# Kernel tuning notes

Hardware: AMD Instinct MI355X
Metric: run time of the kernel (lower is better)

Reference implementation:

```python
import jax, jax.numpy as jnp
import numpy as np

N_EMBD = 512  # scale uses C = n_embd, per original code

def setup_inputs() -> dict:
    key = jax.random.key(0)
    k1, k2, k3, k4 = jax.random.split(key, 4)
    B, T, C, H = 4, 4096, N_EMBD, 64
    x = jax.random.normal(k1, (B, T, C), dtype=jnp.float32)
    # Linear(n_embd, head_size, bias=False); stored as [C, H] for x @ W
    scale = 1.0 / np.sqrt(C)
    Wq = jax.random.normal(k2, (C, H), dtype=jnp.float32) * scale
    Wk = jax.random.normal(k3, (C, H), dtype=jnp.float32) * scale
    Wv = jax.random.normal(k4, (C, H), dtype=jnp.float32) * scale
    return {"x": x, "Wq": Wq, "Wk": Wk, "Wv": Wv}

def reference(x, Wq, Wk, Wv):
    B, T, C = x.shape
    q = jnp.einsum('btc,ch->bth', x, Wq)
    k = jnp.einsum('btc,ch->bth', x, Wk)
    v = jnp.einsum('btc,ch->bth', x, Wv)
    # NOTE: original scales by sqrt(C)=sqrt(n_embd), not sqrt(head_size)
    scores = jnp.einsum('bqh,bkh->bqk', q, k) / jnp.sqrt(jnp.float32(C))
    causal = jnp.tril(jnp.ones((T, T), dtype=bool))
    scores = jnp.where(causal, scores, -jnp.inf)
    weights = jax.nn.softmax(scores, axis=-1)
    out = jnp.einsum('bqk,bkh->bqh', weights, v)
    return out
```

## Files before the change

### kernel.cpp

```cpp
#include <hip/hip_runtime.h>

#define DEV __device__ __forceinline__

typedef __bf16 bf16x8 __attribute__((ext_vector_type(8)));
typedef unsigned short u16x8v __attribute__((ext_vector_type(8)));
typedef float f32x4 __attribute__((ext_vector_type(4)));
typedef float f32x16 __attribute__((ext_vector_type(16)));
typedef unsigned int u32x4v __attribute__((ext_vector_type(4)));
typedef unsigned short u16;
typedef unsigned int u32;

DEV u16 f2bf(float f) {
    u32 u = __builtin_bit_cast(u32, f);
    u = (u + 0x7FFFu + ((u >> 16) & 1u)) >> 16;
    return (u16)u;
}

DEV float bf2f(u16 v) {
    return __builtin_bit_cast(float, (u32)v << 16);
}

DEV bf16x8 ld_bf8(const u16* p) {
    return *reinterpret_cast<const bf16x8*>(p);
}

DEV bf16x8 ld_lds8(const u16* p) {
    ushort4 a = *reinterpret_cast<const ushort4*>(p);
    ushort4 b = *reinterpret_cast<const ushort4*>(p + 4);
    u16x8v o;
    o[0] = a.x; o[1] = a.y; o[2] = a.z; o[3] = a.w;
    o[4] = b.x; o[5] = b.y; o[6] = b.z; o[7] = b.w;
    return __builtin_bit_cast(bf16x8, o);
}

DEV float fexp2(float x) { return __builtin_amdgcn_exp2f(x); }

DEV u32 cvt_pk_bf16(float a, float b) {
    u32 r;
    asm("v_cvt_pk_bf16_f32 %0, %1, %2" : "=v"(r) : "v"(a), "v"(b));
    return r;
}


DEV int block_base(int j) {
    int g = j >> 1, r = j & 1;
    return j + g * (g - 1) + r * g;
}

__global__ __launch_bounds__(256) void prep_kernel(const float* __restrict__ W0,
                                                   const float* __restrict__ W1,
                                                   const float* __restrict__ W2,
                                                   u16* __restrict__ Wt,
                                                   u32* __restrict__ table) {
    const int blk = blockIdx.x;
    if (blk < 384) {
        int idx = blk * 256 + threadIdx.x;
        int w = idx >> 15, rem = idx & 32767, h = rem >> 9, c = rem & 511;
        const float* W = (w == 0) ? W0 : ((w == 1) ? W1 : W2);
        float v = W[c * 64 + h];
        if (w == 0) v *= 0.044194173824159216f * 1.4426950408889634f;
        Wt[idx] = f2bf(v);
    } else {
        int idx = (blk - 384) * 256 + threadIdx.x;
        if (idx < 512) {
            int j = idx >> 4, k = idx & 15;
            if (k <= (j >> 1))
                table[block_base(j) + k] = (u32)j | ((u32)k << 16);
        }
    }
}

__global__ __launch_bounds__(256) void proj_kernel(const float* __restrict__ x,
                                                   const u16* __restrict__ Wt,
                                                   u16* __restrict__ Q,
                                                   u16* __restrict__ Kq,
                                                   u16* __restrict__ Vt) {
    __shared__ __align__(16) u16 xs[64 * 40];
    const int tid = threadIdx.x;
    const int wave = tid >> 6, lane = tid & 63;
    const int lr = lane & 15, lg = lane >> 4;
    const int r0 = blockIdx.x * 64;
    const int srow = tid >> 3, scol = (tid & 7) * 4;

    f32x4 acc[3][4];
#pragma unroll
    for (int m = 0; m < 3; ++m)
#pragma unroll
        for (int b = 0; b < 4; ++b) acc[m][b] = (f32x4){0.f, 0.f, 0.f, 0.f};

    for (int kk = 0; kk < 16; ++kk) {
#pragma unroll
        for (int p = 0; p < 2; ++p) {
            const int row = p * 32 + srow;
            float4 a = *reinterpret_cast<const float4*>(
                x + (size_t)(r0 + row) * 512 + kk * 32 + scol);
            ushort4 hv;
            hv.x = f2bf(a.x); hv.y = f2bf(a.y); hv.z = f2bf(a.z); hv.w = f2bf(a.w);
            *reinterpret_cast<ushort4*>(&xs[row * 40 + scol]) = hv;
        }
        __syncthreads();

        bf16x8 af = ld_bf8(&xs[(wave * 16 + lr) * 40 + lg * 8]);
#pragma unroll
        for (int m = 0; m < 3; ++m) {
#pragma unroll
            for (int nt = 0; nt < 4; ++nt) {
                bf16x8 bf = ld_bf8(Wt + m * 32768 + (lr + 16 * nt) * 512 + kk * 32 + lg * 8);
                acc[m][nt] = __builtin_amdgcn_mfma_f32_16x16x32_bf16(af, bf, acc[m][nt], 0, 0, 0);
            }
        }
        __syncthreads();
    }

    const int rw = r0 + wave * 16;
#pragma unroll
    for (int nt = 0; nt < 4; ++nt) {
        const int h = lr + 16 * nt;
#pragma unroll
        for (int reg = 0; reg < 4; ++reg) {
            Q[(size_t)(rw + 4 * lg + reg) * 64 + h]  = f2bf(acc[0][nt][reg]);
            Kq[(size_t)(rw + 4 * lg + reg) * 64 + h] = f2bf(acc[1][nt][reg]);
        }
    }
    const int bidx = rw >> 12;
    const int t0 = (rw & 4095) + 4 * lg;
#pragma unroll
    for (int nt = 0; nt < 4; ++nt) {
        const int h = lr + 16 * nt;
        ushort4 hv;
        hv.x = f2bf(acc[2][nt][0]); hv.y = f2bf(acc[2][nt][1]);
        hv.z = f2bf(acc[2][nt][2]); hv.w = f2bf(acc[2][nt][3]);
        *reinterpret_cast<ushort4*>(Vt + ((size_t)(bidx * 64 + h)) * 4096 + t0) = hv;
    }
}

DEV void mask_diag(f32x16& st, int q31, int hi) {
#pragma unroll
    for (int reg = 0; reg < 16; ++reg) {
        const int crow = (reg & 3) + 8 * (reg >> 2) + 4 * hi;
        if (crow > q31) st[reg] = -3.0e38f;
    }
}

DEV float max16(const f32x16& a) {
    float m0 = fmaxf(fmaxf(a[0], a[1]), a[2]);
    float m1 = fmaxf(fmaxf(a[3], a[4]), a[5]);
    float m2 = fmaxf(fmaxf(a[6], a[7]), a[8]);
    float m3 = fmaxf(fmaxf(a[9], a[10]), a[11]);
    float m4 = fmaxf(fmaxf(a[12], a[13]), a[14]);
    float m5 = fmaxf(fmaxf(m0, m1), a[15]);
    float m6 = fmaxf(fmaxf(m2, m3), m4);
    return fmaxf(m5, m6);
}

DEV float expsum(f32x16& st, float m) {
    float r0 = 0.f, r1 = 0.f, r2 = 0.f, r3 = 0.f;
#pragma unroll
    for (int g = 0; g < 4; ++g) {
        float p0 = fexp2(st[4 * g + 0] - m);
        float p1 = fexp2(st[4 * g + 1] - m);
        float p2 = fexp2(st[4 * g + 2] - m);
        float p3 = fexp2(st[4 * g + 3] - m);
        st[4 * g + 0] = p0; st[4 * g + 1] = p1;
        st[4 * g + 2] = p2; st[4 * g + 3] = p3;
        r0 += p0; r1 += p1; r2 += p2; r3 += p3;
    }
    return (r0 + r1) + (r2 + r3);
}

DEV void packP(const f32x16& st, bf16x8& pb0, bf16x8& pb1, int hi) {
    u32 A0 = cvt_pk_bf16(st[0], st[1]),  A1 = cvt_pk_bf16(st[2], st[3]);
    u32 A2 = cvt_pk_bf16(st[4], st[5]),  A3 = cvt_pk_bf16(st[6], st[7]);
    u32 A4 = cvt_pk_bf16(st[8], st[9]),  A5 = cvt_pk_bf16(st[10], st[11]);
    u32 A6 = cvt_pk_bf16(st[12], st[13]), A7 = cvt_pk_bf16(st[14], st[15]);
    u32 e0 = __shfl_xor(hi ? A0 : A2, 32, 64);
    u32 e1 = __shfl_xor(hi ? A1 : A3, 32, 64);
    u32 e2 = __shfl_xor(hi ? A4 : A6, 32, 64);
    u32 e3 = __shfl_xor(hi ? A5 : A7, 32, 64);
    u32x4v w0, w1;
    w0[0] = hi ? e0 : A0;
    w0[1] = hi ? e1 : A1;
    w0[2] = hi ? A2 : e0;
    w0[3] = hi ? A3 : e1;
    w1[0] = hi ? e2 : A4;
    w1[1] = hi ? e3 : A5;
    w1[2] = hi ? A6 : e2;
    w1[3] = hi ? A7 : e3;
    pb0 = __builtin_bit_cast(bf16x8, w0);
    pb1 = __builtin_bit_cast(bf16x8, w1);
}

__global__ __launch_bounds__(256) void attn_part_kernel(const u16* __restrict__ Q,
                                                        const u16* __restrict__ K,
                                                        const u16* __restrict__ Vt,
                                                        const u32* __restrict__ table,
                                                        u16* __restrict__ Opart,
                                                        float* __restrict__ Mpart,
                                                        float* __restrict__ Lpart) {
    __shared__ __align__(16) u16 Ks[2][32][68];
    __shared__ __align__(16) u16 Vs[2][64][36];

    const int tid = threadIdx.x;
    const int wave = tid >> 6, lane = tid & 63;
    const int q31 = lane & 31, hi = lane >> 5;
    const int bid = blockIdx.x;
    const int b = bid & 3;
    const u32 e = table[bid >> 2];
    const int j = (int)(e & 0xffff);
    const int c = (int)(e >> 16);
    const int qi = 4 * j + wave;
    const int qr0 = qi * 32;
    const int s0 = c * 8;
    const int s1 = min(4 * j + 4, s0 + 8);
    const int tile = (b << 7) | qi;

    const u16* Qb = Q + (size_t)b * 4096 * 64;
    const u16* Kb = K + (size_t)b * 4096 * 64;
    const u16* Vb = Vt + (size_t)b * 64 * 4096;

    const int kr = tid >> 3, ku = tid & 7;
    const int vd = tid >> 2, vu = tid & 3;
    const u16* ksrc = Kb + (size_t)kr * 64 + ku * 8;
    const u16* vsrc = Vb + (size_t)vd * 4096 + vu * 8;

    bf16x8 qf[4];
#pragma unroll
    for (int kk = 0; kk < 4; ++kk)
        qf[kk] = ld_bf8(Qb + (size_t)(qr0 + q31) * 64 + kk * 16 + hi * 8);

    f32x16 o0, o1;
#pragma unroll
    for (int r = 0; r < 16; ++r) { o0[r] = 0.f; o1[r] = 0.f; }
    float m_run = -1.0e30f, l_run = 0.f;

    ushort4 k0, k1, v0, v1;
    k0 = *reinterpret_cast<const ushort4*>(ksrc + s0 * 2048);
    k1 = *reinterpret_cast<const ushort4*>(ksrc + s0 * 2048 + 4);
    v0 = *reinterpret_cast<const ushort4*>(vsrc + s0 * 32);
    v1 = *reinterpret_cast<const ushort4*>(vsrc + s0 * 32 + 4);
    *reinterpret_cast<ushort4*>(&Ks[0][kr][ku * 8]) = k0;
    *reinterpret_cast<ushort4*>(&Ks[0][kr][ku * 8 + 4]) = k1;
    *reinterpret_cast<ushort4*>(&Vs[0][vd][vu * 8]) = v0;
    *reinterpret_cast<ushort4*>(&Vs[0][vd][vu * 8 + 4]) = v1;
    if (s0 + 1 < s1) {
        k0 = *reinterpret_cast<const ushort4*>(ksrc + (s0 + 1) * 2048);
        k1 = *reinterpret_cast<const ushort4*>(ksrc + (s0 + 1) * 2048 + 4);
        v0 = *reinterpret_cast<const ushort4*>(vsrc + (s0 + 1) * 32);
        v1 = *reinterpret_cast<const ushort4*>(vsrc + (s0 + 1) * 32 + 4);
    }
    __syncthreads();

    for (int s = s0; s < s1; ++s) {
        const int cb = s & 1;
        if (s + 1 < s1) {
            *reinterpret_cast<ushort4*>(&Ks[cb ^ 1][kr][ku * 8]) = k0;
            *reinterpret_cast<ushort4*>(&Ks[cb ^ 1][kr][ku * 8 + 4]) = k1;
            *reinterpret_cast<ushort4*>(&Vs[cb ^ 1][vd][vu * 8]) = v0;
            *reinterpret_cast<ushort4*>(&Vs[cb ^ 1][vd][vu * 8 + 4]) = v1;
        }
        if (s + 2 < s1) {
            k0 = *reinterpret_cast<const ushort4*>(ksrc + (s + 2) * 2048);
            k1 = *reinterpret_cast<const ushort4*>(ksrc + (s + 2) * 2048 + 4);
            v0 = *reinterpret_cast<const ushort4*>(vsrc + (s + 2) * 32);
            v1 = *reinterpret_cast<const ushort4*>(vsrc + (s + 2) * 32 + 4);
        }
        if (s <= qi) {
            f32x16 st;
#pragma unroll
            for (int r = 0; r < 16; ++r) st[r] = 0.f;
#pragma unroll
            for (int kk = 0; kk < 4; ++kk) {
                bf16x8 kf = ld_lds8(&Ks[cb][q31][kk * 16 + hi * 8]);
                st = __builtin_amdgcn_mfma_f32_32x32x16_bf16(kf, qf[kk], st, 0, 0, 0);
            }
            if (s == qi) mask_diag(st, q31, hi);

            float pm = max16(st);
            pm = fmaxf(pm, __shfl_xor(pm, 32, 64));
            if (!__all(pm - m_run <= 11.5f)) {
                float mn = fmaxf(m_run, pm);
                float al = fexp2(m_run - mn);
                m_run = mn;
                l_run *= al;
#pragma unroll
                for (int r = 0; r < 16; ++r) { o0[r] *= al; o1[r] *= al; }
            }
            float rs = expsum(st, m_run);
            rs += __shfl_xor(rs, 32, 64);
            l_run += rs;

            bf16x8 p0, p1;
            packP(st, p0, p1, hi);
            bf16x8 va = ld_lds8(&Vs[cb][q31][hi * 8]);
            bf16x8 vb2 = ld_lds8(&Vs[cb][q31][16 + hi * 8]);
            bf16x8 vc = ld_lds8(&Vs[cb][32 + q31][hi * 8]);
            bf16x8 vdq = ld_lds8(&Vs[cb][32 + q31][16 + hi * 8]);
            o0 = __builtin_amdgcn_mfma_f32_32x32x16_bf16(va, p0, o0, 0, 0, 0);
            o0 = __builtin_amdgcn_mfma_f32_32x32x16_bf16(vb2, p1, o0, 0, 0, 0);
            o1 = __builtin_amdgcn_mfma_f32_32x32x16_bf16(vc, p0, o1, 0, 0, 0);
            o1 = __builtin_amdgcn_mfma_f32_32x32x16_bf16(vdq, p1, o1, 0, 0, 0);
        }
        __syncthreads();
    }

    if (s0 <= qi) {
        const size_t base = (size_t)(tile * 16 + c);
        u16* Op = Opart + base * 2048;
#pragma unroll
        for (int reg = 0; reg < 16; ++reg) {
            const int crow = (reg & 3) + 8 * (reg >> 2) + 4 * hi;
            Op[crow * 32 + q31] = f2bf(o0[reg]);
            Op[(32 + crow) * 32 + q31] = f2bf(o1[reg]);
        }
        if (lane < 32) {
            Mpart[base * 32 + lane] = m_run;
            Lpart[base * 32 + lane] = l_run;
        }
    }
}

__global__ __launch_bounds__(256) void merge_kernel(const u16* __restrict__ Opart,
                                                    const float* __restrict__ Mpart,
                                                    const float* __restrict__ Lpart,
                                                    float* __restrict__ out) {
    __shared__ float ld[2][64 * 33];
    const int tile = blockIdx.x;
    const int tid = threadIdx.x;
    const int q = tid >> 3, dg = tid & 7;
    const int qi = tile & 127;
    const int nkv = qi + 1;
    const int nc = (nkv + 7) >> 3;

    float M = -3.0e38f;
    for (int c = 0; c < nc; ++c)
        M = fmaxf(M, Mpart[(tile * 16 + c) * 32 + q]);

    float L = 0.f;
    float acc[8];
#pragma unroll
    for (int j = 0; j < 8; ++j) acc[j] = 0.f;

    const int drow = tid >> 2;
    const int qq = (tid & 3) * 8;

    u16x8v v = reinterpret_cast<const u16x8v*>(Opart + (size_t)(tile * 16) * 2048)[tid];

    for (int c = 0; c < nc; ++c) {
        const size_t base = (size_t)(tile * 16 + c);
        {
            float* dst = &ld[c & 1][drow * 33 + qq];
#pragma unroll
            for (int j = 0; j < 8; ++j) dst[j] = bf2f(v[j]);
        }
        const int cn = (c + 1 < nc) ? c + 1 : c;
        v = reinterpret_cast<const u16x8v*>(Opart + (size_t)(tile * 16 + cn) * 2048)[tid];

        __syncthreads();
        float w = fexp2(Mpart[base * 32 + q] - M);
        L += w * Lpart[base * 32 + q];
        const float* src = &ld[c & 1][0];
#pragma unroll
        for (int j = 0; j < 8; ++j)
            acc[j] += w * src[(dg * 8 + j) * 33 + q];
    }

    const float inv = 1.0f / L;
    float4 r0, r1;
    r0.x = acc[0] * inv; r0.y = acc[1] * inv; r0.z = acc[2] * inv; r0.w = acc[3] * inv;
    r1.x = acc[4] * inv; r1.y = acc[5] * inv; r1.z = acc[6] * inv; r1.w = acc[7] * inv;
    float4* dst = reinterpret_cast<float4*>(out + ((size_t)(tile * 32 + q)) * 64 + dg * 8);
    dst[0] = r0;
    dst[1] = r1;
}

extern "C" void kernel_launch(void* const* d_in, const int* in_sizes, int n_in,
                              void* d_out, int out_size, void* d_ws, size_t ws_size,
                              hipStream_t stream) {
    const float* x  = (const float*)d_in[0];
    const float* Wq = (const float*)d_in[1];
    const float* Wk = (const float*)d_in[2];
    const float* Wv = (const float*)d_in[3];
    float* out = (float*)d_out;

    char* ws = (char*)d_ws;
    const size_t MB = 1024 * 1024;
    u16* Qw  = (u16*)(ws);
    u16* Kw  = (u16*)(ws + 2 * MB);
    u16* Vtw = (u16*)(ws + 4 * MB);
    u16* Wt  = (u16*)(ws + 6 * MB);
    u32* table = (u32*)(ws + 7 * MB);

    u16* Opart = (u16*)(ws + 8 * MB);
    float* Mpart = (float*)(ws + 8 * MB + 32 * MB);
    float* Lpart = Mpart + (size_t)16 * 512 * 32;

    prep_kernel<<<386, 256, 0, stream>>>(Wq, Wk, Wv, Wt, table);
    proj_kernel<<<256, 256, 0, stream>>>(x, Wt, Qw, Kw, Vtw);
    attn_part_kernel<<<4 * 272, 256, 0, stream>>>(Qw, Kw, Vtw, table, Opart, Mpart, Lpart);
    merge_kernel<<<512, 256, 0, stream>>>(Opart, Mpart, Lpart, out);
}
```

Measured before the change: 74.96 us.

## Double KV chunk size in split attention and stage full x rows in LDS

The attention split-K kernel now covers 16 KV tiles per block instead of 8. Each pipeline step loads and processes two 32-key tiles, with a shared softmax max update per pair. This halves the number of blocks and partials and cuts the number of barriers and the merge work. The projection kernel now stages the whole 64x512 x tile in LDS once, replacing 16 per-step stage/sync rounds, at the cost of much larger LDS use (about 67KB) and lower occupancy. Fewer blocks also mean less parallelism across CUs.

Result: slower. 82.53 us (+10.1%).

```diff
diff --git a/kernel.cpp b/kernel.cpp
--- a/kernel.cpp
+++ b/kernel.cpp
@@ -41,11 +41,6 @@
     return r;
 }
 
-
-DEV int block_base(int j) {
-    int g = j >> 1, r = j & 1;
-    return j + g * (g - 1) + r * g;
-}
 
 __global__ __launch_bounds__(256) void prep_kernel(const float* __restrict__ W0,
                                                    const float* __restrict__ W1,
@@ -64,8 +59,12 @@
         int idx = (blk - 384) * 256 + threadIdx.x;
         if (idx < 512) {
             int j = idx >> 4, k = idx & 15;
-            if (k <= (j >> 1))
-                table[block_base(j) + k] = (u32)j | ((u32)k << 16);
+            int nch = (j >> 2) + 1;
+            if (k < nch) {
+                int base = 0;
+                for (int i = 0; i < j; ++i) base += (i >> 2) + 1;
+                table[base + k] = (u32)j | ((u32)k << 16);
+            }
         }
     }
 }
@@ -75,12 +74,22 @@
                                                    u16* __restrict__ Q,
                                                    u16* __restrict__ Kq,
                                                    u16* __restrict__ Vt) {
-    __shared__ __align__(16) u16 xs[64 * 40];
+    __shared__ __align__(16) u16 xs[64 * 524];
     const int tid = threadIdx.x;
     const int wave = tid >> 6, lane = tid & 63;
     const int lr = lane & 15, lg = lane >> 4;
     const int r0 = blockIdx.x * 64;
-    const int srow = tid >> 3, scol = (tid & 7) * 4;
+
+#pragma unroll
+    for (int p = 0; p < 32; ++p) {
+        const int u = tid + p * 256;
+        const int row = u >> 7, col4 = u & 127;
+        float4 a = *reinterpret_cast<const float4*>(x + (size_t)(r0 + row) * 512 + col4 * 4);
+        ushort4 hv;
+        hv.x = f2bf(a.x); hv.y = f2bf(a.y); hv.z = f2bf(a.z); hv.w = f2bf(a.w);
+        *reinterpret_cast<ushort4*>(&xs[row * 524 + col4 * 4]) = hv;
+    }
+    __syncthreads();
 
     f32x4 acc[3][4];
 #pragma unroll
@@ -89,18 +98,7 @@
         for (int b = 0; b < 4; ++b) acc[m][b] = (f32x4){0.f, 0.f, 0.f, 0.f};
 
     for (int kk = 0; kk < 16; ++kk) {
-#pragma unroll
-        for (int p = 0; p < 2; ++p) {
-            const int row = p * 32 + srow;
-            float4 a = *reinterpret_cast<const float4*>(
-                x + (size_t)(r0 + row) * 512 + kk * 32 + scol);
-            ushort4 hv;
-            hv.x = f2bf(a.x); hv.y = f2bf(a.y); hv.z = f2bf(a.z); hv.w = f2bf(a.w);
-            *reinterpret_cast<ushort4*>(&xs[row * 40 + scol]) = hv;
-        }
-        __syncthreads();
-
-        bf16x8 af = ld_bf8(&xs[(wave * 16 + lr) * 40 + lg * 8]);
+        bf16x8 af = ld_lds8(&xs[(wave * 16 + lr) * 524 + kk * 32 + lg * 8]);
 #pragma unroll
         for (int m = 0; m < 3; ++m) {
 #pragma unroll
@@ -109,7 +107,6 @@
                 acc[m][nt] = __builtin_amdgcn_mfma_f32_16x16x32_bf16(af, bf, acc[m][nt], 0, 0, 0);
             }
         }
-        __syncthreads();
     }
 
     const int rw = r0 + wave * 16;
@@ -197,8 +194,8 @@
                                                         u16* __restrict__ Opart,
                                                         float* __restrict__ Mpart,
                                                         float* __restrict__ Lpart) {
-    __shared__ __align__(16) u16 Ks[2][32][68];
-    __shared__ __align__(16) u16 Vs[2][64][36];
+    __shared__ __align__(16) u16 Ks[2][64][68];
+    __shared__ __align__(16) u16 Vs[2][64][68];
 
     const int tid = threadIdx.x;
     const int wave = tid >> 6, lane = tid & 63;
@@ -210,18 +207,37 @@
     const int c = (int)(e >> 16);
     const int qi = 4 * j + wave;
     const int qr0 = qi * 32;
-    const int s0 = c * 8;
-    const int s1 = min(4 * j + 4, s0 + 8);
+    const int s0 = c * 16;
+    const int s1 = min(4 * j + 4, s0 + 16);
     const int tile = (b << 7) | qi;
 
     const u16* Qb = Q + (size_t)b * 4096 * 64;
     const u16* Kb = K + (size_t)b * 4096 * 64;
     const u16* Vb = Vt + (size_t)b * 64 * 4096;
 
-    const int kr = tid >> 3, ku = tid & 7;
-    const int vd = tid >> 2, vu = tid & 3;
-    const u16* ksrc = Kb + (size_t)kr * 64 + ku * 8;
-    const u16* vsrc = Vb + (size_t)vd * 4096 + vu * 8;
+    const int ur = tid >> 3, uc = (tid & 7) * 8;
+    const u16* ksrc = Kb + (size_t)ur * 64 + uc;
+    const u16* vsrc = Vb + (size_t)ur * 4096 + uc;
+    u16* kdst0 = &Ks[0][ur][uc];
+    u16* vdst0 = &Vs[0][ur][uc];
+    const u16* vsrc1 = Vb + (size_t)(32 + ur) * 4096 + uc;
+    u16* kdst1 = &Ks[0][32 + ur][uc];
+    u16* vdst1 = &Vs[0][32 + ur][uc];
+    const size_t bufstep = (size_t)(&Ks[1][0][0] - &Ks[0][0][0]);
+
+#define LOADPAIR(S)                                                             \
+    {   const int kv = (S) * 2048, tv = (S) * 32;                               \
+        pk0 = *reinterpret_cast<const uint4*>(ksrc + kv);                       \
+        pk1 = *reinterpret_cast<const uint4*>(ksrc + kv + 2048);                \
+        pv0 = *reinterpret_cast<const uint4*>(vsrc + tv);                       \
+        pv1 = *reinterpret_cast<const uint4*>(vsrc1 + tv);  }
+
+#define WRITEBUF(BUF)                                                           \
+    {   const size_t o = (BUF) * bufstep;                                       \
+        *reinterpret_cast<uint4*>(kdst0 + o) = pk0;                             \
+        *reinterpret_cast<uint4*>(kdst1 + o) = pk1;                             \
+        *reinterpret_cast<uint4*>(vdst0 + o) = pv0;                             \
+        *reinterpret_cast<uint4*>(vdst1 + o) = pv1;  }
 
     bf16x8 qf[4];
 #pragma unroll
@@ -233,49 +249,44 @@
     for (int r = 0; r < 16; ++r) { o0[r] = 0.f; o1[r] = 0.f; }
     float m_run = -1.0e30f, l_run = 0.f;
 
-    ushort4 k0, k1, v0, v1;
-    k0 = *reinterpret_cast<const ushort4*>(ksrc + s0 * 2048);
-    k1 = *reinterpret_cast<const ushort4*>(ksrc + s0 * 2048 + 4);
-    v0 = *reinterpret_cast<const ushort4*>(vsrc + s0 * 32);
-    v1 = *reinterpret_cast<const ushort4*>(vsrc + s0 * 32 + 4);
-    *reinterpret_cast<ushort4*>(&Ks[0][kr][ku * 8]) = k0;
-    *reinterpret_cast<ushort4*>(&Ks[0][kr][ku * 8 + 4]) = k1;
-    *reinterpret_cast<ushort4*>(&Vs[0][vd][vu * 8]) = v0;
-    *reinterpret_cast<ushort4*>(&Vs[0][vd][vu * 8 + 4]) = v1;
-    if (s0 + 1 < s1) {
-        k0 = *reinterpret_cast<const ushort4*>(ksrc + (s0 + 1) * 2048);
-        k1 = *reinterpret_cast<const ushort4*>(ksrc + (s0 + 1) * 2048 + 4);
-        v0 = *reinterpret_cast<const ushort4*>(vsrc + (s0 + 1) * 32);
-        v1 = *reinterpret_cast<const ushort4*>(vsrc + (s0 + 1) * 32 + 4);
-    }
+    uint4 pk0, pk1, pv0, pv1;
+    LOADPAIR(s0);
+    WRITEBUF(0);
+    if (s0 + 2 < s1) LOADPAIR(s0 + 2);
     __syncthreads();
 
-    for (int s = s0; s < s1; ++s) {
-        const int cb = s & 1;
-        if (s + 1 < s1) {
-            *reinterpret_cast<ushort4*>(&Ks[cb ^ 1][kr][ku * 8]) = k0;
-            *reinterpret_cast<ushort4*>(&Ks[cb ^ 1][kr][ku * 8 + 4]) = k1;
-            *reinterpret_cast<ushort4*>(&Vs[cb ^ 1][vd][vu * 8]) = v0;
-            *reinterpret_cast<ushort4*>(&Vs[cb ^ 1][vd][vu * 8 + 4]) = v1;
-        }
+    for (int s = s0; s < s1; s += 2) {
+        const int pb = ((s - s0) >> 1) & 1;
         if (s + 2 < s1) {
-            k0 = *reinterpret_cast<const ushort4*>(ksrc + (s + 2) * 2048);
-            k1 = *reinterpret_cast<const ushort4*>(ksrc + (s + 2) * 2048 + 4);
-            v0 = *reinterpret_cast<const ushort4*>(vsrc + (s + 2) * 32);
-            v1 = *reinterpret_cast<const ushort4*>(vsrc + (s + 2) * 32 + 4);
-        }
+            WRITEBUF(pb ^ 1);
+            if (s + 4 < s1) LOADPAIR(s + 4);
+        }
+
         if (s <= qi) {
-            f32x16 st;
-#pragma unroll
-            for (int r = 0; r < 16; ++r) st[r] = 0.f;
+            const bool doB = (s + 1 <= qi);
+            f32x16 stA;
+#pragma unroll
+            for (int r = 0; r < 16; ++r) stA[r] = 0.f;
 #pragma unroll
             for (int kk = 0; kk < 4; ++kk) {
-                bf16x8 kf = ld_lds8(&Ks[cb][q31][kk * 16 + hi * 8]);
-                st = __builtin_amdgcn_mfma_f32_32x32x16_bf16(kf, qf[kk], st, 0, 0, 0);
-            }
-            if (s == qi) mask_diag(st, q31, hi);
-
-            float pm = max16(st);
+                bf16x8 kf = ld_lds8(&Ks[pb][q31][kk * 16 + hi * 8]);
+                stA = __builtin_amdgcn_mfma_f32_32x32x16_bf16(kf, qf[kk], stA, 0, 0, 0);
+            }
+            if (s == qi) mask_diag(stA, q31, hi);
+            f32x16 stB;
+            if (doB) {
+#pragma unroll
+                for (int r = 0; r < 16; ++r) stB[r] = 0.f;
+#pragma unroll
+                for (int kk = 0; kk < 4; ++kk) {
+                    bf16x8 kf = ld_lds8(&Ks[pb][32 + q31][kk * 16 + hi * 8]);
+                    stB = __builtin_amdgcn_mfma_f32_32x32x16_bf16(kf, qf[kk], stB, 0, 0, 0);
+                }
+                if (s + 1 == qi) mask_diag(stB, q31, hi);
+            }
+
+            float pm = max16(stA);
+            if (doB) pm = fmaxf(pm, max16(stB));
             pm = fmaxf(pm, __shfl_xor(pm, 32, 64));
             if (!__all(pm - m_run <= 11.5f)) {
                 float mn = fmaxf(m_run, pm);
@@ -285,23 +296,39 @@
 #pragma unroll
                 for (int r = 0; r < 16; ++r) { o0[r] *= al; o1[r] *= al; }
             }
-            float rs = expsum(st, m_run);
+            float rs = expsum(stA, m_run);
+            if (doB) rs += expsum(stB, m_run);
             rs += __shfl_xor(rs, 32, 64);
             l_run += rs;
 
             bf16x8 p0, p1;
-            packP(st, p0, p1, hi);
-            bf16x8 va = ld_lds8(&Vs[cb][q31][hi * 8]);
-            bf16x8 vb2 = ld_lds8(&Vs[cb][q31][16 + hi * 8]);
-            bf16x8 vc = ld_lds8(&Vs[cb][32 + q31][hi * 8]);
-            bf16x8 vdq = ld_lds8(&Vs[cb][32 + q31][16 + hi * 8]);
-            o0 = __builtin_amdgcn_mfma_f32_32x32x16_bf16(va, p0, o0, 0, 0, 0);
-            o0 = __builtin_amdgcn_mfma_f32_32x32x16_bf16(vb2, p1, o0, 0, 0, 0);
-            o1 = __builtin_amdgcn_mfma_f32_32x32x16_bf16(vc, p0, o1, 0, 0, 0);
-            o1 = __builtin_amdgcn_mfma_f32_32x32x16_bf16(vdq, p1, o1, 0, 0, 0);
+            packP(stA, p0, p1, hi);
+            {
+                bf16x8 va = ld_lds8(&Vs[pb][q31][hi * 8]);
+                bf16x8 vb2 = ld_lds8(&Vs[pb][q31][16 + hi * 8]);
+                bf16x8 vc = ld_lds8(&Vs[pb][32 + q31][hi * 8]);
+                bf16x8 vd = ld_lds8(&Vs[pb][32 + q31][16 + hi * 8]);
+                o0 = __builtin_amdgcn_mfma_f32_32x32x16_bf16(va, p0, o0, 0, 0, 0);
+                o0 = __builtin_amdgcn_mfma_f32_32x32x16_bf16(vb2, p1, o0, 0, 0, 0);
+                o1 = __builtin_amdgcn_mfma_f32_32x32x16_bf16(vc, p0, o1, 0, 0, 0);
+                o1 = __builtin_amdgcn_mfma_f32_32x32x16_bf16(vd, p1, o1, 0, 0, 0);
+            }
+            if (doB) {
+                packP(stB, p0, p1, hi);
+                bf16x8 va = ld_lds8(&Vs[pb][q31][32 + hi * 8]);
+                bf16x8 vb2 = ld_lds8(&Vs[pb][q31][48 + hi * 8]);
+                bf16x8 vc = ld_lds8(&Vs[pb][32 + q31][32 + hi * 8]);
+                bf16x8 vd = ld_lds8(&Vs[pb][32 + q31][48 + hi * 8]);
+                o0 = __builtin_amdgcn_mfma_f32_32x32x16_bf16(va, p0, o0, 0, 0, 0);
+                o0 = __builtin_amdgcn_mfma_f32_32x32x16_bf16(vb2, p1, o0, 0, 0, 0);
+                o1 = __builtin_amdgcn_mfma_f32_32x32x16_bf16(vc, p0, o1, 0, 0, 0);
+                o1 = __builtin_amdgcn_mfma_f32_32x32x16_bf16(vd, p1, o1, 0, 0, 0);
+            }
         }
         __syncthreads();
     }
+#undef LOADPAIR
+#undef WRITEBUF
 
     if (s0 <= qi) {
         const size_t base = (size_t)(tile * 16 + c);
@@ -328,8 +355,7 @@
     const int tid = threadIdx.x;
     const int q = tid >> 3, dg = tid & 7;
     const int qi = tile & 127;
-    const int nkv = qi + 1;
-    const int nc = (nkv + 7) >> 3;
+    const int nc = (qi >> 4) + 1;
 
     float M = -3.0e38f;
     for (int c = 0; c < nc; ++c)
@@ -396,6 +422,6 @@
 
     prep_kernel<<<386, 256, 0, stream>>>(Wq, Wk, Wv, Wt, table);
     proj_kernel<<<256, 256, 0, stream>>>(x, Wt, Qw, Kw, Vtw);
-    attn_part_kernel<<<4 * 272, 256, 0, stream>>>(Qw, Kw, Vtw, table, Opart, Mpart, Lpart);
+    attn_part_kernel<<<4 * 144, 256, 0, stream>>>(Qw, Kw, Vtw, table, Opart, Mpart, Lpart);
     merge_kernel<<<512, 256, 0, stream>>>(Opart, Mpart, Lpart, out);
 }
```
